# Performance work log

Measured on AMD Instinct MI355X. Metric: run time of the kernel, lower is better.

The kernel has to match this reference:

```python
import jax, jax.numpy as jnp
import numpy as np

N_NODES = 100000

def setup_inputs() -> dict:
    key = jax.random.key(0)
    k1, k2, k3, k4 = jax.random.split(key, 4)
    feat = jax.random.normal(k1, (N_NODES, 128), dtype=jnp.float32)
    weight = jax.random.normal(k2, (128, 64), dtype=jnp.float32) * 0.05
    src = jax.random.randint(k3, (600000,), 0, N_NODES, dtype=jnp.int64)
    dst = jax.random.randint(k4, (600000,), 0, N_NODES, dtype=jnp.int64)
    return {"feat": feat, "weight": weight, "src": src, "dst": dst}

def reference(feat, weight, src, dst):
    n = feat.shape[0]
    ones = jnp.ones(src.shape[0], dtype=jnp.float32)
    # out-degree of source nodes (edges leave src), in-degree of dst nodes
    out_deg = jnp.clip(jax.ops.segment_sum(ones, src, num_segments=n), 1.0)
    in_deg = jnp.clip(jax.ops.segment_sum(ones, dst, num_segments=n), 1.0)
    norm_src = (out_deg ** -0.5)[:, None]   # [N,1]
    norm_dst = (in_deg ** -0.5)[:, None]    # [N,1]
    # in_feats (128) > out_feats (64): project first, then aggregate
    h = jnp.matmul(feat, weight) * norm_src              # [N, 64]
    msgs = h[src]                                        # [E, 64] gather
    rst = jax.ops.segment_sum(msgs, dst, num_segments=n)  # [N, 64] scatter-sum
    rst = rst * norm_dst
    return rst
```

## Files before the change

### kernel.cpp

```cpp
#include <hip/hip_runtime.h>
#include <hip/hip_fp16.h>

#define IN_F 128
#define OUT_F 64
#define NB   256
#define BSH  9
#define CAP  3840
#define CHUNK 2048
#define KPF  136
#define KPW  144

using short8  = __attribute__((ext_vector_type(8))) short;
using float4v = __attribute__((ext_vector_type(4))) float;

static __device__ inline unsigned short f2bf(float x) {
    union { float f; unsigned u; } v; v.f = x;
    unsigned r = (v.u + 0x7fffu + ((v.u >> 16) & 1u)) >> 16;
    return (unsigned short)r;
}

__global__ __launch_bounds__(256) void bin_kernel(
    const int* __restrict__ src, const int* __restrict__ dst,
    int* __restrict__ gcur_d, int* __restrict__ gcur_s,
    unsigned* __restrict__ bkt_d, unsigned short* __restrict__ bkt_s, int E)
{
    __shared__ int hd[NB], hs[NB], based[NB], bases[NB];
    const int tid = threadIdx.x;
    const int e0  = blockIdx.x * CHUNK;

    hd[tid] = 0; hs[tid] = 0;
    __syncthreads();

    int sv[8], dv[8];
    #pragma unroll
    for (int j = 0; j < 8; ++j) {
        int i = e0 + j * 256 + tid;
        if (i < E) { sv[j] = src[i]; dv[j] = dst[i]; }
        else       { sv[j] = -1;     dv[j] = -1; }
    }
    #pragma unroll
    for (int j = 0; j < 8; ++j) {
        if (dv[j] >= 0) {
            atomicAdd(&hd[dv[j] >> BSH], 1);
            atomicAdd(&hs[sv[j] >> BSH], 1);
        }
    }
    __syncthreads();

    int cd = hd[tid], cs = hs[tid];
    based[tid] = cd ? atomicAdd(&gcur_d[tid], cd) : 0;
    bases[tid] = cs ? atomicAdd(&gcur_s[tid], cs) : 0;
    hd[tid] = 0; hs[tid] = 0;
    __syncthreads();

    #pragma unroll
    for (int j = 0; j < 8; ++j) {
        if (dv[j] >= 0) {
            int bd = dv[j] >> BSH;
            int pd = atomicAdd(&hd[bd], 1) + based[bd];
            if (pd < CAP)
                bkt_d[(size_t)bd * CAP + pd] =
                    (unsigned)sv[j] | ((unsigned)(dv[j] & 511) << 17);
            int bs = sv[j] >> BSH;
            int ps = atomicAdd(&hs[bs], 1) + bases[bs];
            if (ps < CAP) bkt_s[(size_t)bs * CAP + ps] = (unsigned short)(sv[j] & 511);
        }
    }
}

__global__ __launch_bounds__(256) void base_kernel(const int* __restrict__ gcur_d,
                                                   int* __restrict__ bbase)
{
    __shared__ int sc[256];
    int tid = threadIdx.x;
    int v = gcur_d[tid];
    sc[tid] = v; __syncthreads();
    for (int o = 1; o < 256; o <<= 1) {
        int t = (tid >= o) ? sc[tid - o] : 0;
        __syncthreads();
        sc[tid] += t;
        __syncthreads();
    }
    bbase[tid] = sc[tid] - v;
}

__global__ __launch_bounds__(256) void outdeg_kernel(
    const unsigned short* __restrict__ bkt_s, const int* __restrict__ gcur_s,
    int* __restrict__ outdeg, int n)
{
    __shared__ int hist[512];
    const int b = blockIdx.x, tid = threadIdx.x;
    hist[tid] = 0; hist[tid + 256] = 0;
    __syncthreads();
    const int m = min(gcur_s[b], CAP);
    for (int i = tid; i < m; i += 256)
        atomicAdd(&hist[bkt_s[(size_t)b * CAP + i]], 1);
    __syncthreads();
    int node = b * 512 + tid;
    if (node < n) outdeg[node] = hist[tid];
    node += 256;
    if (node < n) outdeg[node] = hist[tid + 256];
}

__global__ __launch_bounds__(256) void csr_kernel(
    const unsigned* __restrict__ bkt_d, const int* __restrict__ gcur_d,
    const int* __restrict__ bbase, int* __restrict__ off, int* __restrict__ ebuf)
{
    __shared__ int hist[512], curs[512], sc[256];
    __shared__ int sbuf[CAP];
    const int b = blockIdx.x, tid = threadIdx.x;
    const int cnt  = min(gcur_d[b], CAP);
    const int base = bbase[b];

    hist[tid] = 0; hist[tid + 256] = 0;
    __syncthreads();
    for (int i = tid; i < cnt; i += 256)
        atomicAdd(&hist[bkt_d[(size_t)b * CAP + i] >> 17], 1);
    __syncthreads();

    int a0 = hist[2 * tid], a1 = hist[2 * tid + 1];
    int psum = a0 + a1;
    sc[tid] = psum; __syncthreads();
    for (int o = 1; o < 256; o <<= 1) {
        int t = (tid >= o) ? sc[tid - o] : 0;
        __syncthreads();
        sc[tid] += t;
        __syncthreads();
    }
    int excl = sc[tid] - psum;
    curs[2 * tid]     = excl;
    curs[2 * tid + 1] = excl + a0;
    off[b * 512 + 2 * tid]     = base + excl;
    off[b * 512 + 2 * tid + 1] = base + excl + a0;
    __syncthreads();

    for (int i = tid; i < cnt; i += 256) {
        unsigned e = bkt_d[(size_t)b * CAP + i];
        int p = atomicAdd(&curs[e >> 17], 1);
        sbuf[p] = (int)(e & 0x1FFFFu);
    }
    __syncthreads();
    for (int i = tid; i < cnt; i += 256)
        ebuf[base + i] = sbuf[i];
}

__global__ __launch_bounds__(256) void gemm_norm_kernel(
    const float* __restrict__ feat,
    const float* __restrict__ W,
    const int*   __restrict__ outdeg,
    __half* __restrict__ h,
    int n)
{
    __shared__ unsigned short Fh[128 * KPF];
    __shared__ unsigned short Wt[64 * KPW];

    const int tid  = threadIdx.x;
    const int row0 = blockIdx.x * 128;

    {
        const float4* W4 = (const float4*)W;
        #pragma unroll
        for (int it = 0; it < 8; ++it) {
            int i4 = it * 256 + tid;
            int k  = i4 >> 4;
            int c4 = (i4 & 15) * 4;
            float4 wv = W4[i4];
            Wt[(c4 + 0) * KPW + k] = f2bf(wv.x);
            Wt[(c4 + 1) * KPW + k] = f2bf(wv.y);
            Wt[(c4 + 2) * KPW + k] = f2bf(wv.z);
            Wt[(c4 + 3) * KPW + k] = f2bf(wv.w);
        }
    }
    {
        const float4* F4 = (const float4*)feat;
        #pragma unroll
        for (int it = 0; it < 16; ++it) {
            int i4 = it * 256 + tid;
            int r  = i4 >> 5;
            int c4 = (i4 & 31) * 4;
            int gr = row0 + r; if (gr >= n) gr = n - 1;
            float4 v = F4[(long)gr * 32 + (i4 & 31)];
            ushort4 u;
            u.x = f2bf(v.x); u.y = f2bf(v.y); u.z = f2bf(v.z); u.w = f2bf(v.w);
            *(ushort4*)&Fh[r * KPF + c4] = u;
        }
    }
    __syncthreads();

    const int w  = tid >> 6;
    const int l  = tid & 63;
    const int ml = l & 15;
    const int q  = l >> 4;

    float4v acc[2][4];
    #pragma unroll
    for (int rt = 0; rt < 2; ++rt)
        #pragma unroll
        for (int ct = 0; ct < 4; ++ct)
            acc[rt][ct] = (float4v){0.f, 0.f, 0.f, 0.f};

    #pragma unroll
    for (int ks = 0; ks < 4; ++ks) {
        const int ko = ks * 32 + q * 8;
        short8 a0 = *(const short8*)&Fh[(w * 32 +  0 + ml) * KPF + ko];
        short8 a1 = *(const short8*)&Fh[(w * 32 + 16 + ml) * KPF + ko];
        short8 b0 = *(const short8*)&Wt[( 0 + ml) * KPW + ko];
        short8 b1 = *(const short8*)&Wt[(16 + ml) * KPW + ko];
        short8 b2 = *(const short8*)&Wt[(32 + ml) * KPW + ko];
        short8 b3 = *(const short8*)&Wt[(48 + ml) * KPW + ko];
        acc[0][0] = __builtin_amdgcn_mfma_f32_16x16x32_bf16(a0, b0, acc[0][0], 0, 0, 0);
        acc[0][1] = __builtin_amdgcn_mfma_f32_16x16x32_bf16(a0, b1, acc[0][1], 0, 0, 0);
        acc[0][2] = __builtin_amdgcn_mfma_f32_16x16x32_bf16(a0, b2, acc[0][2], 0, 0, 0);
        acc[0][3] = __builtin_amdgcn_mfma_f32_16x16x32_bf16(a0, b3, acc[0][3], 0, 0, 0);
        acc[1][0] = __builtin_amdgcn_mfma_f32_16x16x32_bf16(a1, b0, acc[1][0], 0, 0, 0);
        acc[1][1] = __builtin_amdgcn_mfma_f32_16x16x32_bf16(a1, b1, acc[1][1], 0, 0, 0);
        acc[1][2] = __builtin_amdgcn_mfma_f32_16x16x32_bf16(a1, b2, acc[1][2], 0, 0, 0);
        acc[1][3] = __builtin_amdgcn_mfma_f32_16x16x32_bf16(a1, b3, acc[1][3], 0, 0, 0);
    }

    #pragma unroll
    for (int rt = 0; rt < 2; ++rt) {
        #pragma unroll
        for (int reg = 0; reg < 4; ++reg) {
            int row = row0 + w * 32 + rt * 16 + q * 4 + reg;
            if (row < n) {
                float ns = rsqrtf(fmaxf((float)outdeg[row], 1.0f));
                #pragma unroll
                for (int ct = 0; ct < 4; ++ct)
                    h[(long)row * OUT_F + ct * 16 + ml] = __float2half(acc[rt][ct][reg] * ns);
            }
        }
    }
}

__global__ __launch_bounds__(256) void gather_kernel(
    const int* __restrict__ ebuf, const int* __restrict__ off,
    const __half* __restrict__ h, float* __restrict__ out, int n)
{
    int d  = blockIdx.x * 4 + (threadIdx.x >> 6);
    int l  = threadIdx.x & 63;
    int q  = l >> 4;
    int t  = l & 15;
    if (d >= n) return;
    int beg = off[d], end = off[d + 1];
    int m = end - beg;
    float4 acc = make_float4(0.f, 0.f, 0.f, 0.f);
    int j = beg + q;
    for (; j + 4 < end; j += 8) {
        int s0 = ebuf[j], s1 = ebuf[j + 4];
        __half2 p0 = *(const __half2*)&h[(long)s0 * OUT_F + 4 * t];
        __half2 p1 = *(const __half2*)&h[(long)s0 * OUT_F + 4 * t + 2];
        __half2 p2 = *(const __half2*)&h[(long)s1 * OUT_F + 4 * t];
        __half2 p3 = *(const __half2*)&h[(long)s1 * OUT_F + 4 * t + 2];
        float2 f0 = __half22float2(p0), f1 = __half22float2(p1);
        float2 f2 = __half22float2(p2), f3 = __half22float2(p3);
        acc.x += f0.x + f2.x; acc.y += f0.y + f2.y;
        acc.z += f1.x + f3.x; acc.w += f1.y + f3.y;
    }
    if (j < end) {
        int s = ebuf[j];
        __half2 p0 = *(const __half2*)&h[(long)s * OUT_F + 4 * t];
        __half2 p1 = *(const __half2*)&h[(long)s * OUT_F + 4 * t + 2];
        float2 f0 = __half22float2(p0), f1 = __half22float2(p1);
        acc.x += f0.x; acc.y += f0.y; acc.z += f1.x; acc.w += f1.y;
    }
    acc.x += __shfl_xor(acc.x, 16); acc.y += __shfl_xor(acc.y, 16);
    acc.z += __shfl_xor(acc.z, 16); acc.w += __shfl_xor(acc.w, 16);
    acc.x += __shfl_xor(acc.x, 32); acc.y += __shfl_xor(acc.y, 32);
    acc.z += __shfl_xor(acc.z, 32); acc.w += __shfl_xor(acc.w, 32);
    if (q == 0) {
        float nd = rsqrtf(fmaxf((float)m, 1.0f));
        acc.x *= nd; acc.y *= nd; acc.z *= nd; acc.w *= nd;
        *(float4*)&out[(long)d * OUT_F + 4 * t] = acc;
    }
}

extern "C" void kernel_launch(void* const* d_in, const int* in_sizes, int n_in,
                              void* d_out, int out_size, void* d_ws, size_t ws_size,
                              hipStream_t stream) {
    const float* feat = (const float*)d_in[0];
    const float* W    = (const float*)d_in[1];
    const int*   src  = (const int*)d_in[2];
    const int*   dst  = (const int*)d_in[3];
    float* out = (float*)d_out;

    const int n = in_sizes[0] / IN_F;
    const int E = in_sizes[2];

    char* wsb = (char*)d_ws;
    int* gcur_d = (int*)wsb;
    int* gcur_s = gcur_d + 256;
    int* bbase  = gcur_s + 256;
    int* outdeg = bbase + 256;
    int* off    = outdeg + n;
    size_t pos = (((size_t)(4 * 256 + n + NB * 512 + 1)) * 4 + 15) & ~(size_t)15;
    unsigned* bkt_d = (unsigned*)(wsb + pos);
    pos = (pos + (size_t)NB * CAP * 4 + 15) & ~(size_t)15;
    unsigned short* bkt_s = (unsigned short*)(wsb + pos);
    pos = (pos + (size_t)NB * CAP * 2 + 15) & ~(size_t)15;
    int* ebuf = (int*)(wsb + pos);
    pos = (pos + (size_t)E * 4 + 15) & ~(size_t)15;
    __half* h = (__half*)(wsb + pos);

    hipMemsetAsync(gcur_d, 0, 2 * NB * sizeof(int), stream);

    bin_kernel<<<(E + CHUNK - 1) / CHUNK, 256, 0, stream>>>(src, dst, gcur_d, gcur_s,
                                                            bkt_d, bkt_s, E);
    base_kernel<<<1, 256, 0, stream>>>(gcur_d, bbase);
    outdeg_kernel<<<NB, 256, 0, stream>>>(bkt_s, gcur_s, outdeg, n);
    csr_kernel<<<NB, 256, 0, stream>>>(bkt_d, gcur_d, bbase, off, ebuf);
    gemm_norm_kernel<<<(n + 127) / 128, 256, 0, stream>>>(feat, W, outdeg, h, n);
    gather_kernel<<<(n + 3) / 4, 256, 0, stream>>>(ebuf, off, h, out, n);
}
```

Baseline: 166.1 us.

## Replace global-atomic binning with per-block slices and fuse CSR/outdeg kernels

Binning now writes edges into fixed per-(bucket, block) slices with per-block counts, which removes the memset, the global atomic cursors and the separate base-scan kernel. A single csr_all kernel prefix-sums the slice counts, stages records in LDS, builds the per-bucket CSR with fixed-stride (b*SCAP) offsets stored as (offset, degree) pairs, and computes out-degree in the same pass. The gather kernel switches to 8 edges in flight per row with 16-byte loads per lane. Fixed slice capacity (K_SL=48) and SCAP can silently drop edges if a block's bucket count exceeds it, and the csr kernel uses more LDS, which may lower occupancy.

Result: slower. 182.8 us (+10.1%).

```diff
diff --git a/kernel.cpp b/kernel.cpp
--- a/kernel.cpp
+++ b/kernel.cpp
@@ -3,10 +3,11 @@
 
 #define IN_F 128
 #define OUT_F 64
-#define NB   256
-#define BSH  9
-#define CAP  3840
-#define CHUNK 2048
+#define NB    256
+#define BSH   9
+#define NBLK  256
+#define K_SL  48
+#define SCAP  3840
 #define KPF  136
 #define KPW  144
 
@@ -21,59 +22,54 @@
 
 __global__ __launch_bounds__(256) void bin_kernel(
     const int* __restrict__ src, const int* __restrict__ dst,
-    int* __restrict__ gcur_d, int* __restrict__ gcur_s,
+    int* __restrict__ cnt_d, int* __restrict__ cnt_s,
     unsigned* __restrict__ bkt_d, unsigned short* __restrict__ bkt_s, int E)
 {
-    __shared__ int hd[NB], hs[NB], based[NB], bases[NB];
+    __shared__ int cd[NB], cs[NB];
     const int tid = threadIdx.x;
-    const int e0  = blockIdx.x * CHUNK;
-
-    hd[tid] = 0; hs[tid] = 0;
-    __syncthreads();
-
-    int sv[8], dv[8];
-    #pragma unroll
-    for (int j = 0; j < 8; ++j) {
-        int i = e0 + j * 256 + tid;
-        if (i < E) { sv[j] = src[i]; dv[j] = dst[i]; }
-        else       { sv[j] = -1;     dv[j] = -1; }
-    }
-    #pragma unroll
-    for (int j = 0; j < 8; ++j) {
-        if (dv[j] >= 0) {
-            atomicAdd(&hd[dv[j] >> BSH], 1);
-            atomicAdd(&hs[sv[j] >> BSH], 1);
-        }
-    }
-    __syncthreads();
-
-    int cd = hd[tid], cs = hs[tid];
-    based[tid] = cd ? atomicAdd(&gcur_d[tid], cd) : 0;
-    bases[tid] = cs ? atomicAdd(&gcur_s[tid], cs) : 0;
-    hd[tid] = 0; hs[tid] = 0;
-    __syncthreads();
-
-    #pragma unroll
-    for (int j = 0; j < 8; ++j) {
-        if (dv[j] >= 0) {
-            int bd = dv[j] >> BSH;
-            int pd = atomicAdd(&hd[bd], 1) + based[bd];
-            if (pd < CAP)
-                bkt_d[(size_t)bd * CAP + pd] =
-                    (unsigned)sv[j] | ((unsigned)(dv[j] & 511) << 17);
-            int bs = sv[j] >> BSH;
-            int ps = atomicAdd(&hs[bs], 1) + bases[bs];
-            if (ps < CAP) bkt_s[(size_t)bs * CAP + ps] = (unsigned short)(sv[j] & 511);
-        }
-    }
-}
-
-__global__ __launch_bounds__(256) void base_kernel(const int* __restrict__ gcur_d,
-                                                   int* __restrict__ bbase)
-{
-    __shared__ int sc[256];
-    int tid = threadIdx.x;
-    int v = gcur_d[tid];
+    const int blk = blockIdx.x;
+    const int ch  = (E + NBLK - 1) / NBLK;
+    const int e0  = blk * ch;
+    const int e1  = min(e0 + ch, E);
+
+    cd[tid] = 0; cs[tid] = 0;
+    __syncthreads();
+
+    for (int e = e0 + tid; e < e1; e += 256) {
+        int s = src[e], d = dst[e];
+        int bd = d >> BSH;
+        int pd = atomicAdd(&cd[bd], 1);
+        if (pd < K_SL)
+            bkt_d[((size_t)bd * NBLK + blk) * K_SL + pd] =
+                (unsigned)s | ((unsigned)(d & 511) << 17);
+        int bs = s >> BSH;
+        int ps = atomicAdd(&cs[bs], 1);
+        if (ps < K_SL)
+            bkt_s[((size_t)bs * NBLK + blk) * K_SL + ps] = (unsigned short)(s & 511);
+    }
+    __syncthreads();
+    cnt_d[tid * NBLK + blk] = min(cd[tid], K_SL);
+    cnt_s[tid * NBLK + blk] = min(cs[tid], K_SL);
+}
+
+__global__ __launch_bounds__(256) void csr_all_kernel(
+    const unsigned* __restrict__ bkt_d, const unsigned short* __restrict__ bkt_s,
+    const int* __restrict__ cnt_d, const int* __restrict__ cnt_s,
+    int2* __restrict__ off_deg, int* __restrict__ ebuf, int* __restrict__ outdeg, int n)
+{
+    __shared__ int scnt[NB], sbase[NB], scnt_s[NB], sc[256];
+    __shared__ int hist[512], curs[512], hist_s[512];
+    __shared__ unsigned rec[SCAP];
+    __shared__ int sout[SCAP];
+    const int b = blockIdx.x, tid = threadIdx.x;
+
+    scnt[tid]   = cnt_d[b * NBLK + tid];
+    scnt_s[tid] = cnt_s[b * NBLK + tid];
+    hist[tid] = 0; hist[tid + 256] = 0;
+    hist_s[tid] = 0; hist_s[tid + 256] = 0;
+    __syncthreads();
+
+    int v = scnt[tid];
     sc[tid] = v; __syncthreads();
     for (int o = 1; o < 256; o <<= 1) {
         int t = (tid >= o) ? sc[tid - o] : 0;
@@ -81,41 +77,24 @@
         sc[tid] += t;
         __syncthreads();
     }
-    bbase[tid] = sc[tid] - v;
-}
-
-__global__ __launch_bounds__(256) void outdeg_kernel(
-    const unsigned short* __restrict__ bkt_s, const int* __restrict__ gcur_s,
-    int* __restrict__ outdeg, int n)
-{
-    __shared__ int hist[512];
-    const int b = blockIdx.x, tid = threadIdx.x;
-    hist[tid] = 0; hist[tid + 256] = 0;
-    __syncthreads();
-    const int m = min(gcur_s[b], CAP);
-    for (int i = tid; i < m; i += 256)
-        atomicAdd(&hist[bkt_s[(size_t)b * CAP + i]], 1);
-    __syncthreads();
-    int node = b * 512 + tid;
-    if (node < n) outdeg[node] = hist[tid];
-    node += 256;
-    if (node < n) outdeg[node] = hist[tid + 256];
-}
-
-__global__ __launch_bounds__(256) void csr_kernel(
-    const unsigned* __restrict__ bkt_d, const int* __restrict__ gcur_d,
-    const int* __restrict__ bbase, int* __restrict__ off, int* __restrict__ ebuf)
-{
-    __shared__ int hist[512], curs[512], sc[256];
-    __shared__ int sbuf[CAP];
-    const int b = blockIdx.x, tid = threadIdx.x;
-    const int cnt  = min(gcur_d[b], CAP);
-    const int base = bbase[b];
-
-    hist[tid] = 0; hist[tid + 256] = 0;
-    __syncthreads();
-    for (int i = tid; i < cnt; i += 256)
-        atomicAdd(&hist[bkt_d[(size_t)b * CAP + i] >> 17], 1);
+    sbase[tid] = sc[tid] - v;
+    __syncthreads();
+    const int bcnt = min(sc[255], SCAP);
+
+    for (int r = 0; r < 64; ++r) {
+        int slice = r * 4 + (tid >> 6);
+        int slot  = tid & 63;
+        if (slot < scnt[slice]) {
+            unsigned e = bkt_d[((size_t)b * NBLK + slice) * K_SL + slot];
+            int p = sbase[slice] + slot;
+            if (p < SCAP) rec[p] = e;
+            atomicAdd(&hist[e >> 17], 1);
+        }
+        if (slot < scnt_s[slice]) {
+            unsigned short s = bkt_s[((size_t)b * NBLK + slice) * K_SL + slot];
+            atomicAdd(&hist_s[s], 1);
+        }
+    }
     __syncthreads();
 
     int a0 = hist[2 * tid], a1 = hist[2 * tid + 1];
@@ -130,18 +109,23 @@
     int excl = sc[tid] - psum;
     curs[2 * tid]     = excl;
     curs[2 * tid + 1] = excl + a0;
-    off[b * 512 + 2 * tid]     = base + excl;
-    off[b * 512 + 2 * tid + 1] = base + excl + a0;
-    __syncthreads();
-
-    for (int i = tid; i < cnt; i += 256) {
-        unsigned e = bkt_d[(size_t)b * CAP + i];
+    off_deg[b * 512 + 2 * tid]     = make_int2(b * SCAP + excl,      a0);
+    off_deg[b * 512 + 2 * tid + 1] = make_int2(b * SCAP + excl + a0, a1);
+    __syncthreads();
+
+    for (int i = tid; i < bcnt; i += 256) {
+        unsigned e = rec[i];
         int p = atomicAdd(&curs[e >> 17], 1);
-        sbuf[p] = (int)(e & 0x1FFFFu);
-    }
-    __syncthreads();
-    for (int i = tid; i < cnt; i += 256)
-        ebuf[base + i] = sbuf[i];
+        if (p < SCAP) sout[p] = (int)(e & 0x1FFFFu);
+    }
+    __syncthreads();
+    for (int i = tid; i < bcnt; i += 256)
+        ebuf[b * SCAP + i] = sout[i];
+
+    int node = b * 512 + tid;
+    if (node < n) outdeg[node] = hist_s[tid];
+    node += 256;
+    if (node < n) outdeg[node] = hist_s[tid + 256];
 }
 
 __global__ __launch_bounds__(256) void gemm_norm_kernel(
@@ -234,44 +218,42 @@
 }
 
 __global__ __launch_bounds__(256) void gather_kernel(
-    const int* __restrict__ ebuf, const int* __restrict__ off,
+    const int* __restrict__ ebuf, const int2* __restrict__ off_deg,
     const __half* __restrict__ h, float* __restrict__ out, int n)
 {
-    int d  = blockIdx.x * 4 + (threadIdx.x >> 6);
-    int l  = threadIdx.x & 63;
-    int q  = l >> 4;
-    int t  = l & 15;
+    int d = blockIdx.x * 4 + (threadIdx.x >> 6);
+    int l = threadIdx.x & 63;
+    int o = l >> 3;
+    int t = l & 7;
     if (d >= n) return;
-    int beg = off[d], end = off[d + 1];
-    int m = end - beg;
-    float4 acc = make_float4(0.f, 0.f, 0.f, 0.f);
-    int j = beg + q;
-    for (; j + 4 < end; j += 8) {
-        int s0 = ebuf[j], s1 = ebuf[j + 4];
-        __half2 p0 = *(const __half2*)&h[(long)s0 * OUT_F + 4 * t];
-        __half2 p1 = *(const __half2*)&h[(long)s0 * OUT_F + 4 * t + 2];
-        __half2 p2 = *(const __half2*)&h[(long)s1 * OUT_F + 4 * t];
-        __half2 p3 = *(const __half2*)&h[(long)s1 * OUT_F + 4 * t + 2];
-        float2 f0 = __half22float2(p0), f1 = __half22float2(p1);
-        float2 f2 = __half22float2(p2), f3 = __half22float2(p3);
-        acc.x += f0.x + f2.x; acc.y += f0.y + f2.y;
-        acc.z += f1.x + f3.x; acc.w += f1.y + f3.y;
-    }
-    if (j < end) {
+    int2 od = off_deg[d];
+    int beg = od.x, m = od.y, end = od.x + od.y;
+    float a0 = 0.f, a1 = 0.f, a2 = 0.f, a3 = 0.f;
+    float a4 = 0.f, a5 = 0.f, a6 = 0.f, a7 = 0.f;
+    for (int j = beg + o; j < end; j += 8) {
         int s = ebuf[j];
-        __half2 p0 = *(const __half2*)&h[(long)s * OUT_F + 4 * t];
-        __half2 p1 = *(const __half2*)&h[(long)s * OUT_F + 4 * t + 2];
-        float2 f0 = __half22float2(p0), f1 = __half22float2(p1);
-        acc.x += f0.x; acc.y += f0.y; acc.z += f1.x; acc.w += f1.y;
-    }
-    acc.x += __shfl_xor(acc.x, 16); acc.y += __shfl_xor(acc.y, 16);
-    acc.z += __shfl_xor(acc.z, 16); acc.w += __shfl_xor(acc.w, 16);
-    acc.x += __shfl_xor(acc.x, 32); acc.y += __shfl_xor(acc.y, 32);
-    acc.z += __shfl_xor(acc.z, 32); acc.w += __shfl_xor(acc.w, 32);
-    if (q == 0) {
+        union { uint4 u; __half2 h2[4]; } P;
+        P.u = *(const uint4*)&h[(long)s * OUT_F + 8 * t];
+        float2 f0 = __half22float2(P.h2[0]);
+        float2 f1 = __half22float2(P.h2[1]);
+        float2 f2 = __half22float2(P.h2[2]);
+        float2 f3 = __half22float2(P.h2[3]);
+        a0 += f0.x; a1 += f0.y; a2 += f1.x; a3 += f1.y;
+        a4 += f2.x; a5 += f2.y; a6 += f3.x; a7 += f3.y;
+    }
+    #pragma unroll
+    for (int mask = 8; mask <= 32; mask <<= 1) {
+        a0 += __shfl_xor(a0, mask); a1 += __shfl_xor(a1, mask);
+        a2 += __shfl_xor(a2, mask); a3 += __shfl_xor(a3, mask);
+        a4 += __shfl_xor(a4, mask); a5 += __shfl_xor(a5, mask);
+        a6 += __shfl_xor(a6, mask); a7 += __shfl_xor(a7, mask);
+    }
+    if (o == 0) {
         float nd = rsqrtf(fmaxf((float)m, 1.0f));
-        acc.x *= nd; acc.y *= nd; acc.z *= nd; acc.w *= nd;
-        *(float4*)&out[(long)d * OUT_F + 4 * t] = acc;
+        float4 v0 = make_float4(a0 * nd, a1 * nd, a2 * nd, a3 * nd);
+        float4 v1 = make_float4(a4 * nd, a5 * nd, a6 * nd, a7 * nd);
+        *(float4*)&out[(long)d * OUT_F + 8 * t]     = v0;
+        *(float4*)&out[(long)d * OUT_F + 8 * t + 4] = v1;
     }
 }
 
@@ -288,27 +270,23 @@
     const int E = in_sizes[2];
 
     char* wsb = (char*)d_ws;
-    int* gcur_d = (int*)wsb;
-    int* gcur_s = gcur_d + 256;
-    int* bbase  = gcur_s + 256;
-    int* outdeg = bbase + 256;
-    int* off    = outdeg + n;
-    size_t pos = (((size_t)(4 * 256 + n + NB * 512 + 1)) * 4 + 15) & ~(size_t)15;
+    int* cnt_d  = (int*)wsb;
+    int* cnt_s  = cnt_d + NB * NBLK;
+    int* outdeg = cnt_s + NB * NBLK;
+    size_t pos = (((size_t)(2 * NB * NBLK + n)) * 4 + 15) & ~(size_t)15;
+    int2* off_deg = (int2*)(wsb + pos);
+    pos = (pos + (size_t)NB * 512 * 8 + 15) & ~(size_t)15;
+    int* ebuf = (int*)(wsb + pos);
+    pos = (pos + (size_t)NB * SCAP * 4 + 15) & ~(size_t)15;
     unsigned* bkt_d = (unsigned*)(wsb + pos);
-    pos = (pos + (size_t)NB * CAP * 4 + 15) & ~(size_t)15;
+    pos = (pos + (size_t)NB * NBLK * K_SL * 4 + 15) & ~(size_t)15;
     unsigned short* bkt_s = (unsigned short*)(wsb + pos);
-    pos = (pos + (size_t)NB * CAP * 2 + 15) & ~(size_t)15;
-    int* ebuf = (int*)(wsb + pos);
-    pos = (pos + (size_t)E * 4 + 15) & ~(size_t)15;
+    pos = (pos + (size_t)NB * NBLK * K_SL * 2 + 15) & ~(size_t)15;
     __half* h = (__half*)(wsb + pos);
 
-    hipMemsetAsync(gcur_d, 0, 2 * NB * sizeof(int), stream);
-
-    bin_kernel<<<(E + CHUNK - 1) / CHUNK, 256, 0, stream>>>(src, dst, gcur_d, gcur_s,
-                                                            bkt_d, bkt_s, E);
-    base_kernel<<<1, 256, 0, stream>>>(gcur_d, bbase);
-    outdeg_kernel<<<NB, 256, 0, stream>>>(bkt_s, gcur_s, outdeg, n);
-    csr_kernel<<<NB, 256, 0, stream>>>(bkt_d, gcur_d, bbase, off, ebuf);
+    bin_kernel<<<NBLK, 256, 0, stream>>>(src, dst, cnt_d, cnt_s, bkt_d, bkt_s, E);
+    csr_all_kernel<<<NB, 256, 0, stream>>>(bkt_d, bkt_s, cnt_d, cnt_s,
+                                           off_deg, ebuf, outdeg, n);
     gemm_norm_kernel<<<(n + 127) / 128, 256, 0, stream>>>(feat, W, outdeg, h, n);
-    gather_kernel<<<(n + 3) / 4, 256, 0, stream>>>(ebuf, off, h, out, n);
-}
+    gather_kernel<<<(n + 3) / 4, 256, 0, stream>>>(ebuf, off_deg, h, out, n);
+}
```
